# Performance work log

Hardware: AMD Instinct MI355X
Metric: run time of the kernel (lower is better)

Reference implementation:

```python
import jax, jax.numpy as jnp
import numpy as np

N = 16  # joints (fixed by MM shape 16x8 and MaxPool1d(2))
B = 8192
F_IN = 256
F_OUT = 256
NEG = -9e15


def _build_adj():
    # ring adjacency with self loops: adj[i, i], adj[i, i+-1 mod N]
    A = np.eye(N, dtype=np.float32)
    idx = np.arange(N)
    A[idx, (idx + 1) % N] = 1.0
    A[idx, (idx - 1) % N] = 1.0
    rows, cols = np.nonzero(A)  # row-major order, matches torch adj[m] = e semantics
    return A, rows.astype(np.int32), cols.astype(np.int32)


def setup_inputs() -> dict:
    key = jax.random.key(0)
    k_x, k_w, k_mm, k_b = jax.random.split(key, 4)
    _, rows, cols = _build_adj()
    nnz = rows.shape[0]  # 48
    stdv = 1.0 / np.sqrt(F_OUT)
    return {
        "x": jax.random.normal(k_x, (B, N, F_IN), dtype=jnp.float32),
        "W": jax.random.normal(k_w, (3, F_IN, F_OUT), dtype=jnp.float32)
             * np.sqrt(2.0 / F_IN),  # kaiming-normal scale
        "MM": jax.random.normal(k_mm, (N, 8), dtype=jnp.float32) * np.sqrt(2.0 / N),
        "e": jnp.ones((1, nnz), dtype=jnp.float32),  # init.constant_(1)
        "bias": (jax.random.uniform(k_b, (F_OUT,), dtype=jnp.float32) * 2.0 - 1.0) * stdv,
        "mask_rows": jnp.asarray(rows),
        "mask_cols": jnp.asarray(cols),
    }


def reference(x, W, MM, e, bias, mask_rows, mask_cols):
    # three parallel projections: [B, N, F_out]
    h0 = jnp.einsum("bnf,fg->bng", x, W[0])
    h1 = jnp.einsum("bnf,fg->bng", x, W[1])
    h3 = jnp.einsum("bnf,fg->bng", x, W[2])

    # masked-adjacency attention: scatter learned edge weights, softmax rows
    A = jnp.full((N, N), NEG, dtype=x.dtype).at[mask_rows, mask_cols].set(e[0])
    A = jax.nn.softmax(A, axis=1)
    A = A * (1.0 - jnp.eye(N, dtype=x.dtype))  # zero out self-attention

    out = h0 + jnp.einsum("ij,bjg->big", A, h1)

    # global branch: maxpool joints 16->8, mix back with softmax(MM)
    f_div_C = jax.nn.softmax(MM, axis=1)  # [16, 8]
    Bn, _, G = h3.shape
    h3p = h3.reshape(Bn, N // 2, 2, G).max(axis=2)  # MaxPool1d(k=2) over joints
    y1 = jnp.einsum("ik,bkg->big", f_div_C, h3p)

    out = out + y1 * 0.5
    return out + bias[None, None, :]
```

## Files before the change

kernel.cpp:

```cpp
#include <hip/hip_runtime.h>
#include <hip/hip_fp16.h>
#include <math.h>


typedef _Float16 f16;
typedef _Float16 f16x4 __attribute__((ext_vector_type(4)));
typedef _Float16 f16x8 __attribute__((ext_vector_type(8)));
typedef float f32x4 __attribute__((ext_vector_type(4)));

#define WS_AL 393216
#define WS_AR (393216 + 64)
#define WS_F  (393216 + 128)

#define NEG_BIG (-9e15f)

__global__ __launch_bounds__(256) void prep_kernel(
    const float* __restrict__ W, const float* __restrict__ MM,
    const float* __restrict__ e, const int* __restrict__ rows,
    const int* __restrict__ cols, char* __restrict__ ws)
{
  int bid = blockIdx.x;
  if (bid < 192) {
    __shared__ float t[32][33];
    int m = bid / 64, tile = bid % 64;
    int gi = (tile / 8) * 32, ki = (tile % 8) * 32;
    int tr = threadIdx.x >> 5, tc = threadIdx.x & 31;
    const float* src = W + m * 65536;
    f16* dst = (f16*)ws + m * 65536;
#pragma unroll
    for (int i = 0; i < 4; i++)
      t[tr + 8 * i][tc] = src[(ki + tr + 8 * i) * 256 + gi + tc];
    __syncthreads();
#pragma unroll
    for (int i = 0; i < 4; i++)
      dst[(gi + tr + 8 * i) * 256 + ki + tc] = (f16)t[tc][tr + 8 * i];
  } else {
    __shared__ float Arow[16][17];
    int tid = threadIdx.x;
    if (tid < 16) {
      for (int c = 0; c < 16; c++) Arow[tid][c] = NEG_BIG;
    }
    __syncthreads();
    if (tid < 48) Arow[rows[tid]][cols[tid]] = e[tid];
    __syncthreads();
    if (tid < 16) {
      float mx = -INFINITY;
      for (int c = 0; c < 16; c++) mx = fmaxf(mx, Arow[tid][c]);
      float d = 0.f;
      for (int c = 0; c < 16; c++) d += expf(Arow[tid][c] - mx);
      float al = expf(Arow[tid][(tid + 15) & 15] - mx) / d;
      float ar = expf(Arow[tid][(tid + 1) & 15] - mx) / d;
      ((float*)(ws + WS_AL))[tid] = al;
      ((float*)(ws + WS_AR))[tid] = ar;
    }
    if (tid >= 64 && tid < 80) {
      int i = tid - 64;
      float v[8];
      float mx = -INFINITY;
      for (int k = 0; k < 8; k++) { v[k] = MM[i * 8 + k]; mx = fmaxf(mx, v[k]); }
      float d = 0.f;
      for (int k = 0; k < 8; k++) d += expf(v[k] - mx);
      for (int k = 0; k < 8; k++)
        ((float*)(ws + WS_F))[i * 8 + k] = expf(v[k] - mx) / d;
    }
  }
}

#define XS_STR 40
#define WL_STR 40

__global__ __launch_bounds__(256, 2) void glgc_main(
    const float* __restrict__ x, const float* __restrict__ bias,
    const char* __restrict__ ws, float* __restrict__ out)
{
  __shared__ __align__(16) char smem[40960];
  f16* xs = (f16*)smem;
  f16* xm = (f16*)(smem + 5120);
  f16* wl = (f16*)(smem + 10240);
  float* h3l = (float*)smem;

  const f16* Wt = (const f16*)ws;
  const float* alf = (const float*)(ws + WS_AL);
  const float* arf = (const float*)(ws + WS_AR);
  const float* fm  = (const float*)(ws + WS_F);

  int bid = blockIdx.x;
  int gt = bid & 1, bt = bid >> 1;
  int row0 = bt * 64;
  int g0 = gt * 128;

  int tid = threadIdx.x;
  int w = tid >> 6, lane = tid & 63;
  int lg = lane >> 4, lc = lane & 15;

  int sr = tid >> 2, sq = tid & 3;
  int si = sr & 15;
  int rp = (sr & ~15) | ((si + 15) & 15);
  int rn = (sr & ~15) | ((si + 1) & 15);
  float al_i = alf[si], ar_i = arf[si];
  const float* xg  = x + (row0 + sr) * 256 + sq * 8;
  const float* xgp = x + (row0 + rp) * 256 + sq * 8;
  const float* xgn = x + (row0 + rn) * 256 + sq * 8;
  f16* xs_w = xs + sr * XS_STR + sq * 8;
  f16* xm_w = xm + sr * XS_STR + sq * 8;

  f32x4 accO[4][2] = {};
  f32x4 accH[4][2] = {};

  for (int kc = 0; kc < 8; kc++) {
    int k0 = kc * 32;
    __syncthreads();
#pragma unroll
    for (int j = 0; j < 2; j++) {
      float4 v  = *(const float4*)(xg  + k0 + j * 4);
      float4 vp = *(const float4*)(xgp + k0 + j * 4);
      float4 vn = *(const float4*)(xgn + k0 + j * 4);
      f16x4 sv = {(f16)v.x, (f16)v.y, (f16)v.z, (f16)v.w};
      f16x4 mv = {(f16)(al_i * vp.x + ar_i * vn.x),
                  (f16)(al_i * vp.y + ar_i * vn.y),
                  (f16)(al_i * vp.z + ar_i * vn.z),
                  (f16)(al_i * vp.w + ar_i * vn.w)};
      *(f16x4*)(xs_w + j * 4) = sv;
      *(f16x4*)(xm_w + j * 4) = mv;
    }
#pragma unroll
    for (int t = 0; t < 6; t++) {
      int idx = tid + t * 256;
      int m = idx >> 9, rem = idx & 511;
      int g = rem >> 2, k8 = rem & 3;
      const f16* src = Wt + (m << 16) + (g0 + g) * 256 + k0 + k8 * 8;
      uint4 v = *(const uint4*)src;
      *(uint4*)(wl + m * 5120 + g * WL_STR + k8 * 8) = v;
    }
    __syncthreads();
    f16x8 xa[4], xma[4];
#pragma unroll
    for (int m = 0; m < 4; m++) {
      xa[m]  = *(const f16x8*)(xs + (m * 16 + lc) * XS_STR + lg * 8);
      xma[m] = *(const f16x8*)(xm + (m * 16 + lc) * XS_STR + lg * 8);
    }
    f16x8 wb0[2], wb1[2], wb2[2];
#pragma unroll
    for (int n = 0; n < 2; n++) {
      int gg = w * 32 + n * 16 + lc;
      wb0[n] = *(const f16x8*)(wl + 0 * 5120 + gg * WL_STR + lg * 8);
      wb1[n] = *(const f16x8*)(wl + 1 * 5120 + gg * WL_STR + lg * 8);
      wb2[n] = *(const f16x8*)(wl + 2 * 5120 + gg * WL_STR + lg * 8);
    }
#pragma unroll
    for (int m = 0; m < 4; m++) {
#pragma unroll
      for (int n = 0; n < 2; n++) {
        accO[m][n] = __builtin_amdgcn_mfma_f32_16x16x32_f16(xa[m],  wb0[n], accO[m][n], 0, 0, 0);
        accO[m][n] = __builtin_amdgcn_mfma_f32_16x16x32_f16(xma[m], wb1[n], accO[m][n], 0, 0, 0);
        accH[m][n] = __builtin_amdgcn_mfma_f32_16x16x32_f16(xa[m],  wb2[n], accH[m][n], 0, 0, 0);
      }
    }
  }

  __syncthreads();
#pragma unroll
  for (int m = 0; m < 4; m++) {
#pragma unroll
    for (int n = 0; n < 2; n++) {
      int col = w * 32 + n * 16 + lc;
#pragma unroll
      for (int r = 0; r < 4; r++)
        h3l[(m * 16 + lg * 4 + r) * 132 + col] = accH[m][n][r];
    }
  }
  __syncthreads();

  float fc[4][8];
#pragma unroll
  for (int r = 0; r < 4; r++)
#pragma unroll
    for (int k = 0; k < 8; k++)
      fc[r][k] = fm[(lg * 4 + r) * 8 + k];
  float b0 = bias[g0 + w * 32 + lc];
  float b1 = bias[g0 + w * 32 + 16 + lc];

#pragma unroll
  for (int m = 0; m < 4; m++) {
#pragma unroll
    for (int n = 0; n < 2; n++) {
      int col = w * 32 + n * 16 + lc;
      float p[8];
#pragma unroll
      for (int k = 0; k < 8; k++)
        p[k] = fmaxf(h3l[(m * 16 + 2 * k) * 132 + col],
                     h3l[(m * 16 + 2 * k + 1) * 132 + col]);
      float bb = n ? b1 : b0;
#pragma unroll
      for (int r = 0; r < 4; r++) {
        float y1 = 0.f;
#pragma unroll
        for (int k = 0; k < 8; k++) y1 += fc[r][k] * p[k];
        int grow = row0 + m * 16 + lg * 4 + r;
        out[grow * 256 + g0 + col] = accO[m][n][r] + 0.5f * y1 + bb;
      }
    }
  }
}

extern "C" void kernel_launch(void* const* d_in, const int* in_sizes, int n_in,
                              void* d_out, int out_size, void* d_ws, size_t ws_size,
                              hipStream_t stream) {
  const float* x    = (const float*)d_in[0];
  const float* W    = (const float*)d_in[1];
  const float* MM   = (const float*)d_in[2];
  const float* e    = (const float*)d_in[3];
  const float* bias = (const float*)d_in[4];
  const int* rows   = (const int*)d_in[5];
  const int* cols   = (const int*)d_in[6];
  float* out = (float*)d_out;
  char* ws = (char*)d_ws;

  prep_kernel<<<193, 256, 0, stream>>>(W, MM, e, rows, cols, ws);
  glgc_main<<<4096, 256, 0, stream>>>(x, bias, ws, out);
}
```

Measured before the change: 325.9 us.

## Load weights via global_load_lds, unpad LDS, prepool h3, raise occupancy

Weight tiles now go straight from global memory to LDS with global_load_lds instead of passing through registers. The padded LDS strides are replaced by a dense layout, which shrinks shared memory to 32KB, and launch bounds are raised to allow 4 blocks per SM. The h3 max-pool is done in registers before the LDS store, halving the epilogue LDS traffic, and the k-loop is fully unrolled. The risks are LDS bank conflicts from the unpadded stride-32 rows and register pressure under the tighter occupancy bound.

```diff
diff --git a/kernel.cpp b/kernel.cpp
--- a/kernel.cpp
+++ b/kernel.cpp
@@ -13,6 +13,12 @@
 #define WS_F  (393216 + 128)
 
 #define NEG_BIG (-9e15f)
+
+__device__ __forceinline__ void gload_lds16(const void* g, void* l) {
+  __builtin_amdgcn_global_load_lds(
+      (const __attribute__((address_space(1))) unsigned int*)g,
+      (__attribute__((address_space(3))) unsigned int*)l, 16, 0, 0);
+}
 
 __global__ __launch_bounds__(256) void prep_kernel(
     const float* __restrict__ W, const float* __restrict__ MM,
@@ -66,18 +72,15 @@
   }
 }
 
-#define XS_STR 40
-#define WL_STR 40
-
-__global__ __launch_bounds__(256, 2) void glgc_main(
+__global__ __launch_bounds__(256, 4) void glgc_main(
     const float* __restrict__ x, const float* __restrict__ bias,
     const char* __restrict__ ws, float* __restrict__ out)
 {
-  __shared__ __align__(16) char smem[40960];
+  __shared__ __align__(16) char smem[32768];
   f16* xs = (f16*)smem;
-  f16* xm = (f16*)(smem + 5120);
-  f16* wl = (f16*)(smem + 10240);
-  float* h3l = (float*)smem;
+  f16* xm = (f16*)(smem + 4096);
+  f16* wl = (f16*)(smem + 8192);
+  float* h3p = (float*)smem;
 
   const f16* Wt = (const f16*)ws;
   const float* alf = (const float*)(ws + WS_AL);
@@ -101,51 +104,67 @@
   const float* xg  = x + (row0 + sr) * 256 + sq * 8;
   const float* xgp = x + (row0 + rp) * 256 + sq * 8;
   const float* xgn = x + (row0 + rn) * 256 + sq * 8;
-  f16* xs_w = xs + sr * XS_STR + sq * 8;
-  f16* xm_w = xm + sr * XS_STR + sq * 8;
+  f16* xs_w = xs + tid * 8;
+  f16* xm_w = xm + tid * 8;
+
+  const f16* wsrc[6];
+  f16* wdst[6];
+#pragma unroll
+  for (int t = 0; t < 6; t++) {
+    int idx = tid + t * 256;
+    int m = idx >> 9, rem = idx & 511;
+    int g = rem >> 2, k8 = rem & 3;
+    wsrc[t] = Wt + (m << 16) + (g0 + g) * 256 + k8 * 8;
+    wdst[t] = wl + idx * 8;
+  }
+
+  const f16* xs_r = xs + lc * 32 + lg * 8;
+  const f16* xm_r = xm + lc * 32 + lg * 8;
+  const f16* wb_r = wl + (w * 32 + lc) * 32 + lg * 8;
 
   f32x4 accO[4][2] = {};
   f32x4 accH[4][2] = {};
 
+#pragma unroll
   for (int kc = 0; kc < 8; kc++) {
     int k0 = kc * 32;
     __syncthreads();
 #pragma unroll
-    for (int j = 0; j < 2; j++) {
-      float4 v  = *(const float4*)(xg  + k0 + j * 4);
-      float4 vp = *(const float4*)(xgp + k0 + j * 4);
-      float4 vn = *(const float4*)(xgn + k0 + j * 4);
-      f16x4 sv = {(f16)v.x, (f16)v.y, (f16)v.z, (f16)v.w};
-      f16x4 mv = {(f16)(al_i * vp.x + ar_i * vn.x),
-                  (f16)(al_i * vp.y + ar_i * vn.y),
-                  (f16)(al_i * vp.z + ar_i * vn.z),
-                  (f16)(al_i * vp.w + ar_i * vn.w)};
-      *(f16x4*)(xs_w + j * 4) = sv;
-      *(f16x4*)(xm_w + j * 4) = mv;
-    }
-#pragma unroll
-    for (int t = 0; t < 6; t++) {
-      int idx = tid + t * 256;
-      int m = idx >> 9, rem = idx & 511;
-      int g = rem >> 2, k8 = rem & 3;
-      const f16* src = Wt + (m << 16) + (g0 + g) * 256 + k0 + k8 * 8;
-      uint4 v = *(const uint4*)src;
-      *(uint4*)(wl + m * 5120 + g * WL_STR + k8 * 8) = v;
+    for (int t = 0; t < 6; t++)
+      gload_lds16(wsrc[t] + k0, wdst[t]);
+    {
+      float4 v0 = *(const float4*)(xg + k0);
+      float4 v1 = *(const float4*)(xg + k0 + 4);
+      float4 p0 = *(const float4*)(xgp + k0);
+      float4 p1 = *(const float4*)(xgp + k0 + 4);
+      float4 n0 = *(const float4*)(xgn + k0);
+      float4 n1 = *(const float4*)(xgn + k0 + 4);
+      f16x8 sv = {(f16)v0.x, (f16)v0.y, (f16)v0.z, (f16)v0.w,
+                  (f16)v1.x, (f16)v1.y, (f16)v1.z, (f16)v1.w};
+      f16x8 mv = {(f16)(al_i * p0.x + ar_i * n0.x),
+                  (f16)(al_i * p0.y + ar_i * n0.y),
+                  (f16)(al_i * p0.z + ar_i * n0.z),
+                  (f16)(al_i * p0.w + ar_i * n0.w),
+                  (f16)(al_i * p1.x + ar_i * n1.x),
+                  (f16)(al_i * p1.y + ar_i * n1.y),
+                  (f16)(al_i * p1.z + ar_i * n1.z),
+                  (f16)(al_i * p1.w + ar_i * n1.w)};
+      *(f16x8*)xs_w = sv;
+      *(f16x8*)xm_w = mv;
     }
     __syncthreads();
     f16x8 xa[4], xma[4];
 #pragma unroll
     for (int m = 0; m < 4; m++) {
-      xa[m]  = *(const f16x8*)(xs + (m * 16 + lc) * XS_STR + lg * 8);
-      xma[m] = *(const f16x8*)(xm + (m * 16 + lc) * XS_STR + lg * 8);
+      xa[m]  = *(const f16x8*)(xs_r + m * 512);
+      xma[m] = *(const f16x8*)(xm_r + m * 512);
     }
     f16x8 wb0[2], wb1[2], wb2[2];
 #pragma unroll
     for (int n = 0; n < 2; n++) {
-      int gg = w * 32 + n * 16 + lc;
-      wb0[n] = *(const f16x8*)(wl + 0 * 5120 + gg * WL_STR + lg * 8);
-      wb1[n] = *(const f16x8*)(wl + 1 * 5120 + gg * WL_STR + lg * 8);
-      wb2[n] = *(const f16x8*)(wl + 2 * 5120 + gg * WL_STR + lg * 8);
+      wb0[n] = *(const f16x8*)(wb_r + n * 512);
+      wb1[n] = *(const f16x8*)(wb_r + n * 512 + 4096);
+      wb2[n] = *(const f16x8*)(wb_r + n * 512 + 8192);
     }
 #pragma unroll
     for (int m = 0; m < 4; m++) {
@@ -164,9 +183,8 @@
 #pragma unroll
     for (int n = 0; n < 2; n++) {
       int col = w * 32 + n * 16 + lc;
-#pragma unroll
-      for (int r = 0; r < 4; r++)
-        h3l[(m * 16 + lg * 4 + r) * 132 + col] = accH[m][n][r];
+      h3p[(m * 8 + lg * 2) * 130 + col]     = fmaxf(accH[m][n][0], accH[m][n][1]);
+      h3p[(m * 8 + lg * 2 + 1) * 130 + col] = fmaxf(accH[m][n][2], accH[m][n][3]);
     }
   }
   __syncthreads();
@@ -188,8 +206,7 @@
       float p[8];
 #pragma unroll
       for (int k = 0; k < 8; k++)
-        p[k] = fmaxf(h3l[(m * 16 + 2 * k) * 132 + col],
-                     h3l[(m * 16 + 2 * k + 1) * 132 + col]);
+        p[k] = h3p[(m * 8 + k) * 130 + col];
       float bb = n ? b1 : b0;
 #pragma unroll
       for (int r = 0; r < 4; r++) {
```

Result: slower. 336.5 us (+3.2%).

## Double-buffer weights via direct global-to-LDS loads and apply adjacency after GEMM

Applied to the files above, without the earlier changes.

The main kernel now streams weight tiles into a double-buffered shared-memory region with global_load_lds, prefetching the next K chunk while MFMAs run. It also stages x in larger chunks with fewer barriers. The ring-adjacency mixing is moved from the input side (building a mixed copy of x in each chunk) to the output side, where it is applied to the h1 accumulator through LDS. The maxpool is folded into the h3 spill to LDS. Shared memory grows to 64 KB per block, which may lower occupancy, and there is extra epilogue LDS traffic.

```diff
diff --git a/kernel.cpp b/kernel.cpp
--- a/kernel.cpp
+++ b/kernel.cpp
@@ -4,15 +4,19 @@
 
 
 typedef _Float16 f16;
-typedef _Float16 f16x4 __attribute__((ext_vector_type(4)));
 typedef _Float16 f16x8 __attribute__((ext_vector_type(8)));
 typedef float f32x4 __attribute__((ext_vector_type(4)));
 
 #define WS_AL 393216
 #define WS_AR (393216 + 64)
 #define WS_F  (393216 + 128)
-
 #define NEG_BIG (-9e15f)
+
+__device__ __forceinline__ void gload_lds16(const void* g, void* l) {
+  __builtin_amdgcn_global_load_lds(
+      (const __attribute__((address_space(1))) unsigned int*)g,
+      (__attribute__((address_space(3))) unsigned int*)l, 16, 0, 0);
+}
 
 __global__ __launch_bounds__(256) void prep_kernel(
     const float* __restrict__ W, const float* __restrict__ MM,
@@ -66,18 +70,11 @@
   }
 }
 
-#define XS_STR 40
-#define WL_STR 40
-
 __global__ __launch_bounds__(256, 2) void glgc_main(
     const float* __restrict__ x, const float* __restrict__ bias,
     const char* __restrict__ ws, float* __restrict__ out)
 {
-  __shared__ __align__(16) char smem[40960];
-  f16* xs = (f16*)smem;
-  f16* xm = (f16*)(smem + 5120);
-  f16* wl = (f16*)(smem + 10240);
-  float* h3l = (float*)smem;
+  __shared__ __align__(16) char smem[65536];
 
   const f16* Wt = (const f16*)ws;
   const float* alf = (const float*)(ws + WS_AL);
@@ -94,113 +91,149 @@
   int lg = lane >> 4, lc = lane & 15;
 
   int sr = tid >> 2, sq = tid & 3;
-  int si = sr & 15;
-  int rp = (sr & ~15) | ((si + 15) & 15);
-  int rn = (sr & ~15) | ((si + 1) & 15);
-  float al_i = alf[si], ar_i = arf[si];
-  const float* xg  = x + (row0 + sr) * 256 + sq * 8;
-  const float* xgp = x + (row0 + rp) * 256 + sq * 8;
-  const float* xgn = x + (row0 + rn) * 256 + sq * 8;
-  f16* xs_w = xs + sr * XS_STR + sq * 8;
-  f16* xm_w = xm + sr * XS_STR + sq * 8;
-
-  f32x4 accO[4][2] = {};
-  f32x4 accH[4][2] = {};
-
-  for (int kc = 0; kc < 8; kc++) {
-    int k0 = kc * 32;
-    __syncthreads();
-#pragma unroll
-    for (int j = 0; j < 2; j++) {
-      float4 v  = *(const float4*)(xg  + k0 + j * 4);
-      float4 vp = *(const float4*)(xgp + k0 + j * 4);
-      float4 vn = *(const float4*)(xgn + k0 + j * 4);
-      f16x4 sv = {(f16)v.x, (f16)v.y, (f16)v.z, (f16)v.w};
-      f16x4 mv = {(f16)(al_i * vp.x + ar_i * vn.x),
-                  (f16)(al_i * vp.y + ar_i * vn.y),
-                  (f16)(al_i * vp.z + ar_i * vn.z),
-                  (f16)(al_i * vp.w + ar_i * vn.w)};
-      *(f16x4*)(xs_w + j * 4) = sv;
-      *(f16x4*)(xm_w + j * 4) = mv;
-    }
-#pragma unroll
-    for (int t = 0; t < 6; t++) {
-      int idx = tid + t * 256;
-      int m = idx >> 9, rem = idx & 511;
-      int g = rem >> 2, k8 = rem & 3;
-      const f16* src = Wt + (m << 16) + (g0 + g) * 256 + k0 + k8 * 8;
-      uint4 v = *(const uint4*)src;
-      *(uint4*)(wl + m * 5120 + g * WL_STR + k8 * 8) = v;
-    }
-    __syncthreads();
-    f16x8 xa[4], xma[4];
-#pragma unroll
-    for (int m = 0; m < 4; m++) {
-      xa[m]  = *(const f16x8*)(xs + (m * 16 + lc) * XS_STR + lg * 8);
-      xma[m] = *(const f16x8*)(xm + (m * 16 + lc) * XS_STR + lg * 8);
-    }
+  const float* xrow = x + (row0 + sr) * 256 + sq * 8;
+
+  const f16* wsrc[6];
+  int wdst[6];
+#pragma unroll
+  for (int t = 0; t < 6; ++t) {
+    int idx = tid + t * 256;
+    int m = idx >> 9, rem = idx & 511;
+    int g = rem >> 2, k8 = rem & 3;
+    wsrc[t] = Wt + (m << 16) + (g0 + g) * 256 + k8 * 8;
+    wdst[t] = 16384 + idx * 16;
+  }
+
+  f32x4 acc0[4][2] = {};
+  f32x4 acc1[4][2] = {};
+  f32x4 acc2[4][2] = {};
+
+#pragma unroll
+  for (int t = 0; t < 6; ++t)
+    gload_lds16(wsrc[t], smem + wdst[t]);
+
+#pragma unroll
+  for (int c = 0; c < 8; ++c) {
+    if ((c & 3) == 0) {
+      const float* xb = xrow + (c >> 2) * 128;
+      float4 xv[8];
+#pragma unroll
+      for (int k2 = 0; k2 < 4; ++k2) {
+        xv[2 * k2]     = *(const float4*)(xb + k2 * 32);
+        xv[2 * k2 + 1] = *(const float4*)(xb + k2 * 32 + 4);
+      }
+#pragma unroll
+      for (int k2 = 0; k2 < 4; ++k2) {
+        float4 a = xv[2 * k2], b = xv[2 * k2 + 1];
+        f16x8 v = {(f16)a.x, (f16)a.y, (f16)a.z, (f16)a.w,
+                   (f16)b.x, (f16)b.y, (f16)b.z, (f16)b.w};
+        *(f16x8*)(smem + k2 * 4096 + tid * 16) = v;
+      }
+      asm volatile("s_waitcnt lgkmcnt(0)" ::: "memory");
+    }
+    if (c < 7) {
+#pragma unroll
+      for (int t = 0; t < 6; ++t)
+        gload_lds16(wsrc[t] + (c + 1) * 32, smem + wdst[t] + ((c + 1) & 1) * 24576);
+      asm volatile("s_waitcnt vmcnt(6)" ::: "memory");
+    } else {
+      asm volatile("s_waitcnt vmcnt(0)" ::: "memory");
+    }
+    __builtin_amdgcn_s_barrier();
+    __builtin_amdgcn_sched_barrier(0);
+
+    const char* xcb = smem + (c & 3) * 4096 + lc * 64 + lg * 16;
+    const char* wcb = smem + 16384 + (c & 1) * 24576 + (w * 32 + lc) * 64 + lg * 16;
+    f16x8 xa[4];
+#pragma unroll
+    for (int m = 0; m < 4; ++m) xa[m] = *(const f16x8*)(xcb + m * 1024);
     f16x8 wb0[2], wb1[2], wb2[2];
 #pragma unroll
-    for (int n = 0; n < 2; n++) {
-      int gg = w * 32 + n * 16 + lc;
-      wb0[n] = *(const f16x8*)(wl + 0 * 5120 + gg * WL_STR + lg * 8);
-      wb1[n] = *(const f16x8*)(wl + 1 * 5120 + gg * WL_STR + lg * 8);
-      wb2[n] = *(const f16x8*)(wl + 2 * 5120 + gg * WL_STR + lg * 8);
-    }
-#pragma unroll
-    for (int m = 0; m < 4; m++) {
-#pragma unroll
-      for (int n = 0; n < 2; n++) {
-        accO[m][n] = __builtin_amdgcn_mfma_f32_16x16x32_f16(xa[m],  wb0[n], accO[m][n], 0, 0, 0);
-        accO[m][n] = __builtin_amdgcn_mfma_f32_16x16x32_f16(xma[m], wb1[n], accO[m][n], 0, 0, 0);
-        accH[m][n] = __builtin_amdgcn_mfma_f32_16x16x32_f16(xa[m],  wb2[n], accH[m][n], 0, 0, 0);
-      }
-    }
-  }
-
-  __syncthreads();
-#pragma unroll
-  for (int m = 0; m < 4; m++) {
-#pragma unroll
-    for (int n = 0; n < 2; n++) {
-      int col = w * 32 + n * 16 + lc;
-#pragma unroll
-      for (int r = 0; r < 4; r++)
-        h3l[(m * 16 + lg * 4 + r) * 132 + col] = accH[m][n][r];
+    for (int n = 0; n < 2; ++n) {
+      wb0[n] = *(const f16x8*)(wcb + n * 1024);
+      wb1[n] = *(const f16x8*)(wcb + n * 1024 + 8192);
+      wb2[n] = *(const f16x8*)(wcb + n * 1024 + 16384);
+    }
+#pragma unroll
+    for (int m = 0; m < 4; ++m)
+#pragma unroll
+      for (int n = 0; n < 2; ++n) {
+        acc0[m][n] = __builtin_amdgcn_mfma_f32_16x16x32_f16(xa[m], wb0[n], acc0[m][n], 0, 0, 0);
+        acc1[m][n] = __builtin_amdgcn_mfma_f32_16x16x32_f16(xa[m], wb1[n], acc1[m][n], 0, 0, 0);
+        acc2[m][n] = __builtin_amdgcn_mfma_f32_16x16x32_f16(xa[m], wb2[n], acc2[m][n], 0, 0, 0);
+      }
+    __builtin_amdgcn_sched_barrier(0);
+    __builtin_amdgcn_s_barrier();
+  }
+
+  __syncthreads();
+  float* h1x = (float*)(smem + 16384);
+  int coln0 = w * 32 + lc, coln1 = w * 32 + 16 + lc;
+
+#pragma unroll
+  for (int m = 0; m < 4; ++m)
+#pragma unroll
+    for (int r = 0; r < 4; ++r) {
+      h1x[(m * 16 + lg * 4 + r) * 132 + coln0] = acc1[m][0][r];
+      h1x[(m * 16 + lg * 4 + r) * 132 + coln1] = acc1[m][1][r];
+    }
+  __syncthreads();
+  float alv[4], arv[4];
+#pragma unroll
+  for (int r = 0; r < 4; ++r) {
+    alv[r] = alf[lg * 4 + r];
+    arv[r] = arf[lg * 4 + r];
+  }
+#pragma unroll
+  for (int m = 0; m < 4; ++m)
+#pragma unroll
+    for (int r = 0; r < 4; ++r) {
+      int j = lg * 4 + r;
+      int jm = (j + 15) & 15, jp = (j + 1) & 15;
+      acc0[m][0][r] += alv[r] * h1x[(m * 16 + jm) * 132 + coln0]
+                     + arv[r] * h1x[(m * 16 + jp) * 132 + coln0];
+      acc0[m][1][r] += alv[r] * h1x[(m * 16 + jm) * 132 + coln1]
+                     + arv[r] * h1x[(m * 16 + jp) * 132 + coln1];
+    }
+  __syncthreads();
+
+#pragma unroll
+  for (int m = 0; m < 4; ++m) {
+#pragma unroll
+    for (int n = 0; n < 2; ++n) {
+      int col = n ? coln1 : coln0;
+      h1x[(m * 8 + lg * 2) * 132 + col]     = fmaxf(acc2[m][n][0], acc2[m][n][1]);
+      h1x[(m * 8 + lg * 2 + 1) * 132 + col] = fmaxf(acc2[m][n][2], acc2[m][n][3]);
     }
   }
   __syncthreads();
 
   float fc[4][8];
 #pragma unroll
-  for (int r = 0; r < 4; r++)
-#pragma unroll
-    for (int k = 0; k < 8; k++)
+  for (int r = 0; r < 4; ++r)
+#pragma unroll
+    for (int k = 0; k < 8; ++k)
       fc[r][k] = fm[(lg * 4 + r) * 8 + k];
-  float b0 = bias[g0 + w * 32 + lc];
-  float b1 = bias[g0 + w * 32 + 16 + lc];
-
-#pragma unroll
-  for (int m = 0; m < 4; m++) {
-#pragma unroll
-    for (int n = 0; n < 2; n++) {
-      int col = w * 32 + n * 16 + lc;
+  float bv0 = bias[g0 + coln0], bv1 = bias[g0 + coln1];
+
+#pragma unroll
+  for (int m = 0; m < 4; ++m)
+#pragma unroll
+    for (int n = 0; n < 2; ++n) {
+      int col = n ? coln1 : coln0;
       float p[8];
 #pragma unroll
-      for (int k = 0; k < 8; k++)
-        p[k] = fmaxf(h3l[(m * 16 + 2 * k) * 132 + col],
-                     h3l[(m * 16 + 2 * k + 1) * 132 + col]);
-      float bb = n ? b1 : b0;
-#pragma unroll
-      for (int r = 0; r < 4; r++) {
+      for (int k = 0; k < 8; ++k) p[k] = h1x[(m * 8 + k) * 132 + col];
+      float bb = n ? bv1 : bv0;
+#pragma unroll
+      for (int r = 0; r < 4; ++r) {
         float y1 = 0.f;
 #pragma unroll
-        for (int k = 0; k < 8; k++) y1 += fc[r][k] * p[k];
-        int grow = row0 + m * 16 + lg * 4 + r;
-        out[grow * 256 + g0 + col] = accO[m][n][r] + 0.5f * y1 + bb;
-      }
-    }
-  }
+        for (int k = 0; k < 8; ++k) y1 += fc[r][k] * p[k];
+        out[(row0 + m * 16 + lg * 4 + r) * 256 + g0 + col] =
+            acc0[m][n][r] + 0.5f * y1 + bb;
+      }
+    }
 }
 
 extern "C" void kernel_launch(void* const* d_in, const int* in_sizes, int n_in,
```

New measurement: 286.9 us. -12.0%, faster.
